# Optimization experiments

Measured on AMD Instinct MI355X. Metric: run time of the kernel, lower is better.

## Reference

```python
import jax, jax.numpy as jnp
import numpy as np

MAX_X = 128
B, S, H, D = 2, 512, 8, 64
E = H * D  # embed_dim = 512


def setup_inputs() -> dict:
    key = jax.random.key(0)
    k1, k2, k3 = jax.random.split(key, 3)
    q = jax.random.normal(k1, (B, S, H, D), dtype=jnp.float32)
    embed_table = jax.random.normal(k2, (2 * MAX_X + 1, E), dtype=jnp.float32)
    x = jax.random.randint(k3, (B, S), 0, MAX_X, dtype=jnp.int64)
    return {"q": q, "embed_table": embed_table, "x": x, "max_x": MAX_X}


def reference(q, embed_table, x, max_x):
    # rel[b, i, j] = max_x + x[b, j] - x[b, i]  (faithful to x.reshape(-1,1,S) - x.reshape(-1,S,1))
    rel = max_x + x[:, None, :] - x[:, :, None]          # [B, S, S] int
    rel_e = embed_table[rel]                              # [B, S, S, E] gather
    b, s = rel.shape[0], rel.shape[1]
    h, d = q.shape[2], q.shape[3]
    rel_e = rel_e.reshape(b, s, s, h, d)                  # [B, Sq, Sk, H, D]
    # scores[b, h, q, k] = sum_d q[b, q, h, d] * rel_e[b, q, k, h, d]
    return jnp.einsum('bqhd,bqkhd->bhqk', q, rel_e)
```

## Files before the change

kernel.cpp:

```cpp
#include <hip/hip_runtime.h>
#include <hip/hip_bf16.h>


#define S_LEN 512
#define NH 8
#define HD 64
#define EDIM 512
#define TI 16
#define NR 256
#define TIP 18

typedef __attribute__((ext_vector_type(8))) short bf16x8;
typedef __attribute__((ext_vector_type(4))) float f32x4;

__device__ __forceinline__ ushort2 pk_bf16(float a, float b) {
    union { __hip_bfloat162 h; ushort2 u; } v;
    v.h = __float22bfloat162_rn(float2{a, b});
    return v.u;
}

__global__ __launch_bounds__(256) void relpos_kernel(
    const float* __restrict__ q,
    const float* __restrict__ et,
    const int*   __restrict__ x,
    const int*   __restrict__ maxx_p,
    float*       __restrict__ out)
{
    const int tid = threadIdx.x;
    const int per = S_LEN / TI;
    const int b   = blockIdx.x / (NH * per);
    const int h   = (blockIdx.x / per) % NH;
    const int i0  = (blockIdx.x % per) * TI;

    __shared__ unsigned short Tl[NR * HD];
    __shared__ float          Ts[NR][TIP];
    __shared__ int            xi_s[TI];

    const int w    = tid >> 6;
    const int l    = tid & 63;
    const int quad = l >> 4;
    const int c    = l & 15;

    const float* qrow = q + (((size_t)b * S_LEN + i0 + c) * NH + h) * HD;
    const float4 qa0 = *(const float4*)(qrow + quad * 8);
    const float4 qa1 = *(const float4*)(qrow + quad * 8 + 4);
    const float4 qb0 = *(const float4*)(qrow + 32 + quad * 8);
    const float4 qb1 = *(const float4*)(qrow + 32 + quad * 8 + 4);

    const int rrow = tid >> 4;
    const int c4   = tid & 15;
    const int c8   = c4 >> 1;
    const int half = c4 & 1;
    #pragma unroll
    for (int it = 0; it < 16; ++it) {
        const int r = it * 16 + rrow;
        const float4 v = *(const float4*)(et + (size_t)r * EDIM + h * HD + c4 * 4);
        const ushort2 u0 = pk_bf16(v.x, v.y);
        const ushort2 u1 = pk_bf16(v.z, v.w);
        ushort4 u; u.x = u0.x; u.y = u0.y; u.z = u1.x; u.w = u1.y;
        *(ushort4*)(Tl + r * HD + ((c8 ^ (r & 7)) * 8) + half * 4) = u;
    }

    if (tid < TI) xi_s[tid] = x[b * S_LEN + i0 + tid];
    const int2 xj = *(const int2*)(x + b * S_LEN + 2 * tid);
    const int maxx = maxx_p[0];

    union { bf16x8 v; ushort2 u[4]; } a0u, a1u;
    a0u.u[0] = pk_bf16(qa0.x, qa0.y); a0u.u[1] = pk_bf16(qa0.z, qa0.w);
    a0u.u[2] = pk_bf16(qa1.x, qa1.y); a0u.u[3] = pk_bf16(qa1.z, qa1.w);
    a1u.u[0] = pk_bf16(qb0.x, qb0.y); a1u.u[1] = pk_bf16(qb0.z, qb0.w);
    a1u.u[2] = pk_bf16(qb1.x, qb1.y); a1u.u[3] = pk_bf16(qb1.z, qb1.w);

    __syncthreads();

    f32x4 acc[4];
    #pragma unroll
    for (int nt = 0; nt < 4; ++nt) acc[nt] = (f32x4){0.f, 0.f, 0.f, 0.f};

    #pragma unroll
    for (int nt = 0; nt < 4; ++nt) {
        const int r  = w * 64 + nt * 16 + c;
        const int p0 = quad ^ (c & 7);
        const int p1 = (4 + quad) ^ (c & 7);
        const bf16x8 b0 = *(const bf16x8*)(Tl + r * HD + p0 * 8);
        const bf16x8 b1 = *(const bf16x8*)(Tl + r * HD + p1 * 8);
        acc[nt] = __builtin_amdgcn_mfma_f32_16x16x32_bf16(a0u.v, b0, acc[nt], 0, 0, 0);
        acc[nt] = __builtin_amdgcn_mfma_f32_16x16x32_bf16(a1u.v, b1, acc[nt], 0, 0, 0);
    }

    #pragma unroll
    for (int nt = 0; nt < 4; ++nt) {
        const int r = w * 64 + nt * 16 + c;
        *(float2*)&Ts[r][quad * 4]     = float2{acc[nt][0], acc[nt][1]};
        *(float2*)&Ts[r][quad * 4 + 2] = float2{acc[nt][2], acc[nt][3]};
    }

    __syncthreads();

    float* obase = out + (((size_t)b * NH + h) * S_LEN + i0) * S_LEN;
    #pragma unroll
    for (int ii = 0; ii < TI; ii += 2) {
        const int r0 = (maxx + xj.x - xi_s[ii]) & 255;
        const int r1 = (maxx + xj.y - xi_s[ii]) & 255;
        const int r0b = (maxx + xj.x - xi_s[ii + 1]) & 255;
        const int r1b = (maxx + xj.y - xi_s[ii + 1]) & 255;
        const float2 g0 = *(const float2*)&Ts[r0][ii];
        const float2 g1 = *(const float2*)&Ts[r1][ii];
        float2 o0, o1;
        o0.x = g0.x;
        o0.y = g1.x;
        o1.x = (r0b == r0) ? g0.y : Ts[r0b][ii + 1];
        o1.y = (r1b == r1) ? g1.y : Ts[r1b][ii + 1];
        *(float2*)(obase + (size_t)ii * S_LEN + 2 * tid)       = o0;
        *(float2*)(obase + (size_t)(ii + 1) * S_LEN + 2 * tid) = o1;
    }
}

extern "C" void kernel_launch(void* const* d_in, const int* in_sizes, int n_in,
                              void* d_out, int out_size, void* d_ws, size_t ws_size,
                              hipStream_t stream) {
    const float* q    = (const float*)d_in[0];
    const float* et   = (const float*)d_in[1];
    const int*   x    = (const int*)d_in[2];
    const int*   maxx = (const int*)d_in[3];
    float*       out  = (float*)d_out;

    const int B = in_sizes[2] / S_LEN;
    dim3 grid(B * NH * (S_LEN / TI));
    relpos_kernel<<<grid, 256, 0, stream>>>(q, et, x, maxx, out);
}
```

Measured before the change: 67.82 us.

## Load embedding B-fragments directly into registers and widen output stores to float4

The kernel no longer stages the bf16-converted embedding slice in shared memory. Each lane now loads its MFMA B-operand rows straight from global memory into registers and packs them to bf16 there, which removes an LDS write/read round trip and a barrier. The output phase is also reorganised so each thread writes one float4 per row: half the block covers each of two rows, replacing the paired float2 stores. The trade-off is higher register pressure from holding 16 float4 values per thread, and less coalesced global reads of the table.

```diff
diff --git a/kernel.cpp b/kernel.cpp
--- a/kernel.cpp
+++ b/kernel.cpp
@@ -19,6 +19,13 @@
     return v.u;
 }
 
+__device__ __forceinline__ bf16x8 pack8(float4 lo, float4 hi) {
+    union { bf16x8 v; ushort2 u[4]; } r;
+    r.u[0] = pk_bf16(lo.x, lo.y); r.u[1] = pk_bf16(lo.z, lo.w);
+    r.u[2] = pk_bf16(hi.x, hi.y); r.u[3] = pk_bf16(hi.z, hi.w);
+    return r.v;
+}
+
 __global__ __launch_bounds__(256) void relpos_kernel(
     const float* __restrict__ q,
     const float* __restrict__ et,
@@ -32,60 +39,46 @@
     const int h   = (blockIdx.x / per) % NH;
     const int i0  = (blockIdx.x % per) * TI;
 
-    __shared__ unsigned short Tl[NR * HD];
-    __shared__ float          Ts[NR][TIP];
-    __shared__ int            xi_s[TI];
+    __shared__ float Ts[NR][TIP];
+    __shared__ int   xi_s[TI];
 
     const int w    = tid >> 6;
     const int l    = tid & 63;
     const int quad = l >> 4;
     const int c    = l & 15;
 
-    const float* qrow = q + (((size_t)b * S_LEN + i0 + c) * NH + h) * HD;
-    const float4 qa0 = *(const float4*)(qrow + quad * 8);
-    const float4 qa1 = *(const float4*)(qrow + quad * 8 + 4);
-    const float4 qb0 = *(const float4*)(qrow + 32 + quad * 8);
-    const float4 qb1 = *(const float4*)(qrow + 32 + quad * 8 + 4);
+    const float* qrow = q + (((size_t)b * S_LEN + i0 + c) * NH + h) * HD + quad * 8;
+    const float4 qa0 = *(const float4*)(qrow);
+    const float4 qa1 = *(const float4*)(qrow + 4);
+    const float4 qb0 = *(const float4*)(qrow + 32);
+    const float4 qb1 = *(const float4*)(qrow + 36);
 
-    const int rrow = tid >> 4;
-    const int c4   = tid & 15;
-    const int c8   = c4 >> 1;
-    const int half = c4 & 1;
+    float4 tb[16];
     #pragma unroll
-    for (int it = 0; it < 16; ++it) {
-        const int r = it * 16 + rrow;
-        const float4 v = *(const float4*)(et + (size_t)r * EDIM + h * HD + c4 * 4);
-        const ushort2 u0 = pk_bf16(v.x, v.y);
-        const ushort2 u1 = pk_bf16(v.z, v.w);
-        ushort4 u; u.x = u0.x; u.y = u0.y; u.z = u1.x; u.w = u1.y;
-        *(ushort4*)(Tl + r * HD + ((c8 ^ (r & 7)) * 8) + half * 4) = u;
+    for (int nt = 0; nt < 4; ++nt) {
+        const float* trow = et + (size_t)(w * 64 + nt * 16 + c) * EDIM + h * HD + quad * 8;
+        tb[nt * 4 + 0] = *(const float4*)(trow);
+        tb[nt * 4 + 1] = *(const float4*)(trow + 4);
+        tb[nt * 4 + 2] = *(const float4*)(trow + 32);
+        tb[nt * 4 + 3] = *(const float4*)(trow + 36);
     }
 
     if (tid < TI) xi_s[tid] = x[b * S_LEN + i0 + tid];
-    const int2 xj = *(const int2*)(x + b * S_LEN + 2 * tid);
+    const int4 xj4 = *(const int4*)(x + b * S_LEN + 4 * (tid & 127));
     const int maxx = maxx_p[0];
 
-    union { bf16x8 v; ushort2 u[4]; } a0u, a1u;
-    a0u.u[0] = pk_bf16(qa0.x, qa0.y); a0u.u[1] = pk_bf16(qa0.z, qa0.w);
-    a0u.u[2] = pk_bf16(qa1.x, qa1.y); a0u.u[3] = pk_bf16(qa1.z, qa1.w);
-    a1u.u[0] = pk_bf16(qb0.x, qb0.y); a1u.u[1] = pk_bf16(qb0.z, qb0.w);
-    a1u.u[2] = pk_bf16(qb1.x, qb1.y); a1u.u[3] = pk_bf16(qb1.z, qb1.w);
-
-    __syncthreads();
+    const bf16x8 a0 = pack8(qa0, qa1);
+    const bf16x8 a1 = pack8(qb0, qb1);
 
     f32x4 acc[4];
     #pragma unroll
-    for (int nt = 0; nt < 4; ++nt) acc[nt] = (f32x4){0.f, 0.f, 0.f, 0.f};
-
-    #pragma unroll
     for (int nt = 0; nt < 4; ++nt) {
-        const int r  = w * 64 + nt * 16 + c;
-        const int p0 = quad ^ (c & 7);
-        const int p1 = (4 + quad) ^ (c & 7);
-        const bf16x8 b0 = *(const bf16x8*)(Tl + r * HD + p0 * 8);
-        const bf16x8 b1 = *(const bf16x8*)(Tl + r * HD + p1 * 8);
-        acc[nt] = __builtin_amdgcn_mfma_f32_16x16x32_bf16(a0u.v, b0, acc[nt], 0, 0, 0);
-        acc[nt] = __builtin_amdgcn_mfma_f32_16x16x32_bf16(a1u.v, b1, acc[nt], 0, 0, 0);
+        const bf16x8 b0 = pack8(tb[nt * 4 + 0], tb[nt * 4 + 1]);
+        const bf16x8 b1 = pack8(tb[nt * 4 + 2], tb[nt * 4 + 3]);
+        f32x4 a = (f32x4){0.f, 0.f, 0.f, 0.f};
+        a = __builtin_amdgcn_mfma_f32_16x16x32_bf16(a0, b0, a, 0, 0, 0);
+        a = __builtin_amdgcn_mfma_f32_16x16x32_bf16(a1, b1, a, 0, 0, 0);
+        acc[nt] = a;
     }
 
     #pragma unroll
@@ -98,21 +91,18 @@
     __syncthreads();
 
     float* obase = out + (((size_t)b * NH + h) * S_LEN + i0) * S_LEN;
+    const int jg     = (tid & 127) * 4;
+    const int rowsel = tid >> 7;
     #pragma unroll
     for (int ii = 0; ii < TI; ii += 2) {
-        const int r0 = (maxx + xj.x - xi_s[ii]) & 255;
-        const int r1 = (maxx + xj.y - xi_s[ii]) & 255;
-        const int r0b = (maxx + xj.x - xi_s[ii + 1]) & 255;
-        const int r1b = (maxx + xj.y - xi_s[ii + 1]) & 255;
-        const float2 g0 = *(const float2*)&Ts[r0][ii];
-        const float2 g1 = *(const float2*)&Ts[r1][ii];
-        float2 o0, o1;
-        o0.x = g0.x;
-        o0.y = g1.x;
-        o1.x = (r0b == r0) ? g0.y : Ts[r0b][ii + 1];
-        o1.y = (r1b == r1) ? g1.y : Ts[r1b][ii + 1];
-        *(float2*)(obase + (size_t)ii * S_LEN + 2 * tid)       = o0;
-        *(float2*)(obase + (size_t)(ii + 1) * S_LEN + 2 * tid) = o1;
+        const int row = ii + rowsel;
+        const int xi  = xi_s[row];
+        float4 o;
+        o.x = Ts[(maxx + xj4.x - xi) & 255][row];
+        o.y = Ts[(maxx + xj4.y - xi) & 255][row];
+        o.z = Ts[(maxx + xj4.z - xi) & 255][row];
+        o.w = Ts[(maxx + xj4.w - xi) & 255][row];
+        *(float4*)(obase + (size_t)row * S_LEN + jg) = o;
     }
 }
 
```

Result: slower. 69.78 us (+2.9%).

## Prefetch embed rows to registers, widen output stores to float4, pad Ts to odd stride

Applied to the files above, without the earlier changes.

All sixteen embed-table float4 loads are now issued up front into registers, so their latency overlaps the q and x loads before the bf16 conversion and LDS writes. The output phase changes so each thread writes one float4 per row (half the block per row) instead of float2 pairs. The Ts padding drops to 17 to cut LDS bank conflicts on the scattered reads, at the cost of scalar stores into Ts. Launch bounds ask for 2 blocks per SM, which the 64-float register prefetch may put under pressure.

```diff
diff --git a/kernel.cpp b/kernel.cpp
--- a/kernel.cpp
+++ b/kernel.cpp
@@ -8,7 +8,7 @@
 #define EDIM 512
 #define TI 16
 #define NR 256
-#define TIP 18
+#define TIP 17
 
 typedef __attribute__((ext_vector_type(8))) short bf16x8;
 typedef __attribute__((ext_vector_type(4))) float f32x4;
@@ -19,7 +19,7 @@
     return v.u;
 }
 
-__global__ __launch_bounds__(256) void relpos_kernel(
+__global__ __launch_bounds__(256, 2) void relpos_kernel(
     const float* __restrict__ q,
     const float* __restrict__ et,
     const int*   __restrict__ x,
@@ -40,6 +40,17 @@
     const int l    = tid & 63;
     const int quad = l >> 4;
     const int c    = l & 15;
+    const int rrow = tid >> 4;
+    const int c4   = tid & 15;
+    const int c8   = c4 >> 1;
+    const int half = c4 & 1;
+
+    float4 tv[16];
+    #pragma unroll
+    for (int it = 0; it < 16; ++it) {
+        const int r = it * 16 + rrow;
+        tv[it] = *(const float4*)(et + (size_t)r * EDIM + h * HD + c4 * 4);
+    }
 
     const float* qrow = q + (((size_t)b * S_LEN + i0 + c) * NH + h) * HD;
     const float4 qa0 = *(const float4*)(qrow + quad * 8);
@@ -47,23 +58,18 @@
     const float4 qb0 = *(const float4*)(qrow + 32 + quad * 8);
     const float4 qb1 = *(const float4*)(qrow + 32 + quad * 8 + 4);
 
-    const int rrow = tid >> 4;
-    const int c4   = tid & 15;
-    const int c8   = c4 >> 1;
-    const int half = c4 & 1;
+    if (tid < TI) xi_s[tid] = x[b * S_LEN + i0 + tid];
+    const int4 xj4 = *(const int4*)(x + b * S_LEN + 4 * (tid & 127));
+    const int maxx = maxx_p[0];
+
     #pragma unroll
     for (int it = 0; it < 16; ++it) {
         const int r = it * 16 + rrow;
-        const float4 v = *(const float4*)(et + (size_t)r * EDIM + h * HD + c4 * 4);
-        const ushort2 u0 = pk_bf16(v.x, v.y);
-        const ushort2 u1 = pk_bf16(v.z, v.w);
+        const ushort2 u0 = pk_bf16(tv[it].x, tv[it].y);
+        const ushort2 u1 = pk_bf16(tv[it].z, tv[it].w);
         ushort4 u; u.x = u0.x; u.y = u0.y; u.z = u1.x; u.w = u1.y;
         *(ushort4*)(Tl + r * HD + ((c8 ^ (r & 7)) * 8) + half * 4) = u;
     }
-
-    if (tid < TI) xi_s[tid] = x[b * S_LEN + i0 + tid];
-    const int2 xj = *(const int2*)(x + b * S_LEN + 2 * tid);
-    const int maxx = maxx_p[0];
 
     union { bf16x8 v; ushort2 u[4]; } a0u, a1u;
     a0u.u[0] = pk_bf16(qa0.x, qa0.y); a0u.u[1] = pk_bf16(qa0.z, qa0.w);
@@ -91,28 +97,27 @@
     #pragma unroll
     for (int nt = 0; nt < 4; ++nt) {
         const int r = w * 64 + nt * 16 + c;
-        *(float2*)&Ts[r][quad * 4]     = float2{acc[nt][0], acc[nt][1]};
-        *(float2*)&Ts[r][quad * 4 + 2] = float2{acc[nt][2], acc[nt][3]};
+        Ts[r][quad * 4 + 0] = acc[nt][0];
+        Ts[r][quad * 4 + 1] = acc[nt][1];
+        Ts[r][quad * 4 + 2] = acc[nt][2];
+        Ts[r][quad * 4 + 3] = acc[nt][3];
     }
 
     __syncthreads();
 
     float* obase = out + (((size_t)b * NH + h) * S_LEN + i0) * S_LEN;
+    const int jg     = (tid & 127) * 4;
+    const int rowsel = tid >> 7;
     #pragma unroll
     for (int ii = 0; ii < TI; ii += 2) {
-        const int r0 = (maxx + xj.x - xi_s[ii]) & 255;
-        const int r1 = (maxx + xj.y - xi_s[ii]) & 255;
-        const int r0b = (maxx + xj.x - xi_s[ii + 1]) & 255;
-        const int r1b = (maxx + xj.y - xi_s[ii + 1]) & 255;
-        const float2 g0 = *(const float2*)&Ts[r0][ii];
-        const float2 g1 = *(const float2*)&Ts[r1][ii];
-        float2 o0, o1;
-        o0.x = g0.x;
-        o0.y = g1.x;
-        o1.x = (r0b == r0) ? g0.y : Ts[r0b][ii + 1];
-        o1.y = (r1b == r1) ? g1.y : Ts[r1b][ii + 1];
-        *(float2*)(obase + (size_t)ii * S_LEN + 2 * tid)       = o0;
-        *(float2*)(obase + (size_t)(ii + 1) * S_LEN + 2 * tid) = o1;
+        const int row = ii + rowsel;
+        const int xi  = xi_s[row];
+        float4 o;
+        o.x = Ts[(maxx + xj4.x - xi) & 255][row];
+        o.y = Ts[(maxx + xj4.y - xi) & 255][row];
+        o.z = Ts[(maxx + xj4.z - xi) & 255][row];
+        o.w = Ts[(maxx + xj4.w - xi) & 255][row];
+        *(float4*)(obase + (size_t)row * S_LEN + jg) = o;
     }
 }
 
```

New measurement: 67.83 us. No clear change (+0.0%).
